# Kernel tuning notes

Measured on AMD Instinct MI355X. Metric: run time of the kernel, lower is better.

The kernel has to match this reference:

```python
import jax, jax.numpy as jnp
import numpy as np

# ---- production-scale dims ----
U, I, D = 51200, 25600, 64          # users, items, embed_size
E, EP = 1_000_000, 100_000          # train edges, pos/neg scoring edges
K = 8                               # topk similar users (FFT filter length)
NF = K // 2 + 1                     # rfft bins
CL_BS = 256                         # contrastive chunk size (U % CL_BS == 0)
TEMP = 0.2                          # args.temperature
N_LAYERS = 2                        # args.layers


def setup_inputs() -> dict:
    key = jax.random.key(0)
    ks = jax.random.split(key, 14)
    return {
        "user_emb": jax.random.normal(ks[0], (U, D), jnp.float32) * 0.1,
        "item_emb": jax.random.normal(ks[1], (I, D), jnp.float32) * 0.1,
        "W": jax.random.normal(ks[2], (D, D), jnp.float32) * (1.0 / np.sqrt(D)),
        "a": jax.random.normal(ks[3], (D,), jnp.float32) * 0.1,
        "WU": jax.random.normal(ks[4], (D, D), jnp.float32) * (1.0 / np.sqrt(D)),
        "aU": jax.random.normal(ks[5], (2 * D,), jnp.float32) * 0.1,
        "complex_weight": jax.random.normal(ks[6], (1, NF, D, 2), jnp.float32) * 0.02,
        "rate_src": jax.random.randint(ks[7], (E,), 0, U),
        "rate_dst": jax.random.randint(ks[8], (E,), 0, I),
        "pos_u": jax.random.randint(ks[9], (EP,), 0, U),
        "pos_i": jax.random.randint(ks[10], (EP,), 0, I),
        "neg_u": jax.random.randint(ks[11], (EP,), 0, U),
        "neg_i": jax.random.randint(ks[12], (EP,), 0, I),
        "nbr_idx": jax.random.randint(ks[13], (U, K), 0, U),
    }


def _propagate(src_feat, src_idx, dst_idx, n_dst):
    """DGRecLayer: degree-normalized mean aggregation over bipartite edges."""
    msg = src_feat[src_idx]                                       # [E, D] gather
    agg = jax.ops.segment_sum(msg, dst_idx, num_segments=n_dst)   # [n_dst, D] scatter
    deg = jax.ops.segment_sum(jnp.ones((src_idx.shape[0],), src_feat.dtype),
                              dst_idx, num_segments=n_dst)
    return agg / jnp.maximum(deg, 1.0)[:, None]


def _layer_attention(ls, W, a):
    t = jnp.stack(ls, axis=0)                                     # [L+1, N, D]
    alpha = jax.nn.softmax(jnp.einsum('lnd,de,e->ln', t, W, a), axis=0)
    return jnp.einsum('lnd,ln->nd', t, alpha)


def _anchor_user_embed(user_emb, WU, aU, complex_weight, nbr_idx):
    # Original detaches user embeddings to numpy for the FAISS path.
    ue = jax.lax.stop_gradient(user_emb)
    simu = ue[nbr_idx]                                            # [U, K, D]
    x = jnp.fft.rfft(simu, axis=1, norm='ortho')                  # [U, NF, D]
    wc = complex_weight[..., 0] + 1j * complex_weight[..., 1]     # [1, NF, D]
    simu = jnp.fft.irfft(x * wc, n=K, axis=1, norm='ortho')       # [U, K, D]
    Wsimu = jnp.einsum('ukd,de->uke', simu, WU)                   # [U, K, D]
    Wu = jnp.broadcast_to((ue @ WU)[:, None, :], Wsimu.shape)     # [U, K, D]
    e = jnp.concatenate([Wsimu, Wu], axis=2) @ aU                 # [U, K]
    e = jnp.where(e > 0, e, 0.1 * e)                              # LeakyReLU(0.1)
    alpha = jax.nn.softmax(e, axis=1)
    return jnp.einsum('uke,uk->ue', Wsimu, alpha)                 # [U, D]


def _chunk_contrast(r1, r2):
    B = r1.shape[0]
    n1 = jnp.linalg.norm(r1, axis=-1, keepdims=True)
    n2 = jnp.linalg.norm(r2, axis=-1, keepdims=True)
    s11 = (r1 @ r1.T) / (n1 @ n1.T + 1e-6) / TEMP
    c12 = (r1 @ r2.T) / (n1 @ n2.T + 1e-6) / TEMP
    s22 = (r2 @ r2.T) / (n2 @ n2.T + 1e-6) / TEMP
    c21 = (r2 @ r1.T) / (n2 @ n1.T + 1e-6) / TEMP
    mask = jax.nn.one_hot(jnp.arange(B), 2 * B, dtype=r1.dtype) * (-1e10)
    logits = jnp.concatenate(
        [jnp.concatenate([s11, c12], axis=-1) + mask,
         jnp.concatenate([s22, c21], axis=-1) + mask], axis=0)     # [2B, 2B]
    labels = jnp.concatenate([jnp.arange(B) + B, jnp.arange(B) + B])
    logz = jax.scipy.special.logsumexp(logits, axis=-1)
    return logz - logits[jnp.arange(2 * B), labels]                # per-example CE


def reference(user_emb, item_emb, W, a, WU, aU, complex_weight,
              rate_src, rate_dst, pos_u, pos_i, neg_u, neg_i, nbr_idx):
    h_u, h_i = user_emb, item_emb
    users, items = [h_u], [h_i]
    for _ in range(N_LAYERS):
        new_i = _propagate(h_u, rate_src, rate_dst, I)   # user -> item ('rate')
        new_u = _propagate(h_i, rate_dst, rate_src, U)   # item -> user ('rated by')
        h_u, h_i = new_u, new_i
        users.append(h_u)
        items.append(h_i)
    hu = _layer_attention(users, W, a)                   # [U, D]
    hi = _layer_attention(items, W, a)                   # [I, D]

    anchor = _anchor_user_embed(user_emb, WU, aU, complex_weight, nbr_idx)
    r1 = hu.reshape(-1, CL_BS, D)
    r2 = anchor.reshape(-1, CL_BS, D)
    loss_contrast = jax.vmap(_chunk_contrast)(r1, r2).mean()

    score_pos = jnp.sum(hu[pos_u] * hi[pos_i], axis=-1, keepdims=True)  # u_dot_v
    score_neg = jnp.sum(hu[neg_u] * hi[neg_i], axis=-1, keepdims=True)
    return score_pos, score_neg, loss_contrast
```

## Files before the change

kernel.cpp:

```cpp
#include <hip/hip_runtime.h>
#include <hip/hip_bf16.h>

constexpr int U_  = 51200;
constexpr int I_  = 25600;
constexpr int E_  = 1000000;
constexpr int EP_ = 100000;
constexpr int CB_ = 256;
constexpr int NCHUNK_ = U_ / CB_;
constexpr size_t UD_ = (size_t)U_ * 64;
constexpr size_t ID_ = (size_t)I_ * 64;
constexpr int NBK_ = 200;
constexpr int CAP_ = 8192;
constexpr int TILE_ = 4096;
constexpr int NBA_ = (E_ + TILE_ - 1) / TILE_;
constexpr int NANC_ = U_ / 16;
constexpr int NCVT_ = (int)((UD_ + ID_) / (8 * 256));
constexpr int NSCB_ = (2 * EP_) / 16;

constexpr float SCALE_E_  = 16.f;
constexpr float ISCALE_E_ = 1.f / 16.f;
constexpr float SCALE_1_  = 64.f;
constexpr float ISCALE_1_ = 1.f / 64.f;

constexpr size_t OFF_LOSS  = 0;
constexpr size_t OFF_FLAG  = 1;
constexpr size_t OFF_CURU  = 8;
constexpr size_t OFF_CURI  = 208;
constexpr size_t OFF_VEC   = 448;
constexpr size_t OFF_ROWU  = 1088;
constexpr size_t OFF_ROWI  = ((OFF_ROWU + U_ + 1 + 63) / 64) * 64;
constexpr size_t OFF_CSRU  = ((OFF_ROWI + I_ + 1 + 63) / 64) * 64;
constexpr size_t OFF_CSRI  = OFF_CSRU + E_;
constexpr size_t OFF_U1    = ((OFF_CSRI + E_ + 63) / 64) * 64;
constexpr size_t OFF_I1    = OFF_U1 + UD_;
constexpr size_t OFF_HU    = OFF_I1 + ID_;
constexpr size_t OFF_HI    = OFF_HU + UD_;
constexpr size_t OFF_ANC   = OFF_HI + ID_;
constexpr size_t OFF_UE8   = OFF_ANC + UD_;
constexpr size_t OFF_IE8   = OFF_UE8 + UD_ / 4;
constexpr size_t OFF_U18   = OFF_IE8 + ID_ / 4;
constexpr size_t OFF_I18   = OFF_U18 + UD_ / 4;

#define DEVI static __device__ __forceinline__

typedef _Float16 h2v __attribute__((ext_vector_type(2)));
typedef _Float16 f16x8 __attribute__((ext_vector_type(8)));
typedef float floatx4 __attribute__((ext_vector_type(4)));
typedef unsigned short u16x8 __attribute__((ext_vector_type(8)));

DEVI float b2f(__hip_bfloat16 x) { return __bfloat162float(x); }

DEVI float bfb2f(unsigned short b) {
  unsigned u = ((unsigned)b) << 16; float f; __builtin_memcpy(&f, &u, 4); return f;
}

DEVI float ldf(const void* p, size_t i, int isf32) {
  if (isf32) return ((const float*)p)[i];
  return b2f(((const __hip_bfloat16*)p)[i]);
}

DEVI float frcp(float x) { return __builtin_amdgcn_rcpf(x); }

DEVI float fexp2(float x) {
#if __has_builtin(__builtin_amdgcn_exp2f)
  return __builtin_amdgcn_exp2f(x);
#else
  return exp2f(x);
#endif
}

DEVI float fp8_dec(unsigned v) {
#if __has_builtin(__builtin_amdgcn_cvt_f32_fp8)
  return __builtin_amdgcn_cvt_f32_fp8(v, 0);
#else
  unsigned b = v & 0xFF;
  if (!(b & 0x78)) return 0.f;
  unsigned short h = (unsigned short)(((b & 0x80) << 8) | (((b & 0x7f) + (8 << 3)) << 7));
  _Float16 hf; __builtin_memcpy(&hf, &h, 2);
  return (float)hf;
#endif
}

#if __has_builtin(__builtin_amdgcn_cvt_f32_fp8)
#define FP8D(w, s) __builtin_amdgcn_cvt_f32_fp8((w), (s))
#else
#define FP8D(w, s) fp8_dec(((w) >> (8 * (s))) & 0xFF)
#endif

DEVI unsigned fp8_enc_pk(float a, float b) {
#if __has_builtin(__builtin_amdgcn_cvt_pk_fp8_f32)
  return __builtin_amdgcn_cvt_pk_fp8_f32(a, b, 0u, false);
#else
  auto enc1 = [](float f) -> unsigned {
    _Float16 hf = (_Float16)f; unsigned short hb; __builtin_memcpy(&hb, &hf, 2);
    int s = hb >> 15, e = (hb >> 10) & 31, m = hb & 1023;
    int e8 = e - 15 + 7;
    int m3 = (m + ((1 << 6) + ((m >> 7) & 1))) >> 7;
    if (m3 > 7) { m3 = 0; e8++; }
    if (e8 <= 0) return (unsigned)(s << 7);
    if (e8 > 15) { e8 = 15; m3 = 6; }
    return (unsigned)((s << 7) | (e8 << 3) | m3);
  };
  return enc1(a) | (enc1(b) << 8);
#endif
}

DEVI int waveInclScan(int v, int lane) {
  #pragma unroll
  for (int off = 1; off < 64; off <<= 1) {
    int t = __shfl_up(v, off, 64);
    if (lane >= off) v += t;
  }
  return v;
}

__global__ void prep_kernel(const unsigned short* __restrict__ ueu,
                            const void* __restrict__ W, const void* __restrict__ a,
                            const void* __restrict__ WU, const void* __restrict__ aU,
                            float* __restrict__ vecs, float* __restrict__ flag,
                            float* __restrict__ ws0) {
  int tid = threadIdx.x;
  for (int i = tid; i < 408; i += 256)
    if (i == 0 || i >= 8) ws0[i] = 0.f;
  if (tid < 64) {
    int cnt = 0;
    for (int i = 0; i < 256; i++) {
      int e = (ueu[i] >> 7) & 0xFF;
      if (e >= 130) cnt++;
    }
    int isf32 = (cnt >= 8);
    if (tid == 0) *flag = isf32 ? 1.0f : 0.0f;
    int d = tid;
    float s = 0.f, t1 = 0.f, t2 = 0.f;
    for (int e = 0; e < 64; e++) {
      s += ldf(W, d * 64 + e, isf32) * ldf(a, e, isf32);
      float wue = ldf(WU, d * 64 + e, isf32);
      t1 += wue * ldf(aU, e, isf32);
      t2 += wue * ldf(aU, 64 + e, isf32);
    }
    vecs[d] = s;
    vecs[64 + d] = t1;
    vecs[128 + d] = t2;
  }
}

struct BktSmem {
  int histU[NBK_], histI[NBK_];
  int loffU[NBK_ + 1], loffI[NBK_ + 1];
  int cbU[NBK_], cbI[NBK_];
  int lcU[NBK_], lcI[NBK_];
  int wsU[4], wsI[4];
  unsigned recsU[TILE_], recsI[TILE_];
};
constexpr int WS_ = 72;
struct AncSmem {
  _Float16 WUt[64 * WS_];
  _Float16 mixS[16 * WS_];
  float invSe[16];
  int nbrS[128];
};
constexpr size_t FSA_SMEM = sizeof(BktSmem) > sizeof(AncSmem) ? sizeof(BktSmem) : sizeof(AncSmem);

DEVI void bucketA_body(char* smemRaw, int blk,
    const int* __restrict__ rs, const int* __restrict__ rd,
    unsigned* __restrict__ bufU, unsigned* __restrict__ bufI,
    int* __restrict__ curU, int* __restrict__ curI) {
  BktSmem& S = *(BktSmem*)smemRaw;
  int tid = threadIdx.x;
  int base = blk * TILE_;
  for (int i = tid; i < NBK_; i += 256) { S.histU[i] = 0; S.histI[i] = 0; }
  __syncthreads();
  int ss[16], dd[16];
  #pragma unroll
  for (int t = 0; t < 16; t++) {
    int e = base + t * 256 + tid;
    bool v = e < E_;
    ss[t] = v ? rs[e] : -1;
    dd[t] = v ? rd[e] : 0;
    if (v) {
      atomicAdd(&S.histU[ss[t] >> 8], 1);
      atomicAdd(&S.histI[dd[t] >> 7], 1);
    }
  }
  __syncthreads();
  if (tid < NBK_) {
    int cU = S.histU[tid];
    S.cbU[tid] = tid * CAP_ + (cU ? atomicAdd(&curU[tid], cU) : 0);
    int cI = S.histI[tid];
    S.cbI[tid] = tid * CAP_ + (cI ? atomicAdd(&curI[tid], cI) : 0);
  }
  int lane = tid & 63, wv = tid >> 6;
  int cvU = (tid < NBK_) ? S.histU[tid] : 0;
  int cvI = (tid < NBK_) ? S.histI[tid] : 0;
  int inU = waveInclScan(cvU, lane);
  int inI = waveInclScan(cvI, lane);
  if (lane == 63) { S.wsU[wv] = inU; S.wsI[wv] = inI; }
  __syncthreads();
  int woU = 0, woI = 0;
  for (int w = 0; w < wv; w++) { woU += S.wsU[w]; woI += S.wsI[w]; }
  if (tid < NBK_) {
    S.loffU[tid] = woU + inU - cvU;
    S.loffI[tid] = woI + inI - cvI;
  }
  if (tid == NBK_ - 1) {
    S.loffU[NBK_] = woU + inU;
    S.loffI[NBK_] = woI + inI;
  }
  __syncthreads();
  if (tid < NBK_) { S.lcU[tid] = S.loffU[tid]; S.lcI[tid] = S.loffI[tid]; }
  __syncthreads();
  #pragma unroll
  for (int t = 0; t < 16; t++) {
    if (ss[t] >= 0) {
      int b = ss[t] >> 8;
      int p = atomicAdd(&S.lcU[b], 1);
      S.recsU[p] = ((unsigned)(ss[t] & 255) << 17) | (unsigned)dd[t];
      b = dd[t] >> 7;
      p = atomicAdd(&S.lcI[b], 1);
      S.recsI[p] = ((unsigned)(dd[t] & 127) << 17) | (unsigned)ss[t];
    }
  }
  __syncthreads();
  int totU = S.loffU[NBK_];
  for (int p = tid; p < totU; p += 256) {
    int lo = 0, hi = NBK_;
    while (hi - lo > 1) { int mid = (lo + hi) >> 1; if (S.loffU[mid] <= p) lo = mid; else hi = mid; }
    bufU[S.cbU[lo] + (p - S.loffU[lo])] = S.recsU[p];
  }
  int totI = S.loffI[NBK_];
  for (int p = tid; p < totI; p += 256) {
    int lo = 0, hi = NBK_;
    while (hi - lo > 1) { int mid = (lo + hi) >> 1; if (S.loffI[mid] <= p) lo = mid; else hi = mid; }
    bufI[S.cbI[lo] + (p - S.loffI[lo])] = S.recsI[p];
  }
}

DEVI void anchor_body(char* smemRaw, int blk,
    const void* __restrict__ ue, const void* __restrict__ WU,
    const void* __restrict__ cw, const float* __restrict__ vecs,
    const int* __restrict__ nbr, float* __restrict__ out, int isf32) {
  AncSmem& S = *(AncSmem*)smemRaw;
  int tid = threadIdx.x;
  int wv = tid >> 6, lane = tid & 63;
  int ublk = blk * 16;

  #pragma unroll
  for (int it = 0; it < 16; it++) {
    int k = it * 4 + wv;
    S.WUt[lane * WS_ + k] = (_Float16)ldf(WU, (size_t)k * 64 + lane, isf32);
  }
  if (tid < 128) S.nbrS[tid] = nbr[ublk * 8 + tid];
  __syncthreads();

  float cw0 = ldf(cw, (0 * 64 + lane) * 2, isf32);
  float w1r = ldf(cw, (1 * 64 + lane) * 2, isf32), w1i = ldf(cw, (1 * 64 + lane) * 2 + 1, isf32);
  float w2r = ldf(cw, (2 * 64 + lane) * 2, isf32), w2i = ldf(cw, (2 * 64 + lane) * 2 + 1, isf32);
  float w3r = ldf(cw, (3 * 64 + lane) * 2, isf32), w3i = ldf(cw, (3 * 64 + lane) * 2 + 1, isf32);
  float cw4 = ldf(cw, (4 * 64 + lane) * 2, isf32);
  float v1 = vecs[64 + lane], v2 = vecs[128 + lane];
  const float c1 = 0.70710678118654752440f;

  bool b3 = (lane & 8) != 0, b4 = (lane & 16) != 0, b5 = (lane & 32) != 0;

  float qv0 = ldf(ue, (size_t)(ublk + wv * 4 + 0) * 64 + lane, isf32) * v2;
  float qv1 = ldf(ue, (size_t)(ublk + wv * 4 + 1) * 64 + lane, isf32) * v2;
  float qv2 = ldf(ue, (size_t)(ublk + wv * 4 + 2) * 64 + lane, isf32) * v2;
  float qv3 = ldf(ue, (size_t)(ublk + wv * 4 + 3) * 64 + lane, isf32) * v2;
  qv0 += __shfl_xor(qv0, 16, 64); qv0 += __shfl_xor(qv0, 32, 64);
  qv1 += __shfl_xor(qv1, 16, 64); qv1 += __shfl_xor(qv1, 32, 64);
  qv2 += __shfl_xor(qv2, 16, 64); qv2 += __shfl_xor(qv2, 32, 64);
  qv3 += __shfl_xor(qv3, 16, 64); qv3 += __shfl_xor(qv3, 32, 64);
  float qs0 = b4 ? qv1 : qv0;
  float qs1 = b4 ? qv3 : qv2;
  float qw = b5 ? qs1 : qs0;
  qw += __shfl_xor(qw, 1, 64); qw += __shfl_xor(qw, 2, 64);
  qw += __shfl_xor(qw, 4, 64); qw += __shfl_xor(qw, 8, 64);

  float xc[8], xn[8];
  #pragma unroll
  for (int k = 0; k < 8; k++)
    xc[k] = ldf(ue, (size_t)S.nbrS[wv * 32 + k] * 64 + lane, isf32);

  for (int u4 = 0; u4 < 4; u4++) {
    int uL = wv * 4 + u4;
    if (u4 < 3) {
      #pragma unroll
      for (int k = 0; k < 8; k++)
        xn[k] = ldf(ue, (size_t)S.nbrS[wv * 32 + (u4 + 1) * 8 + k] * 64 + lane, isf32);
    }
    float sA = xc[1] - xc[3] - xc[5] + xc[7];
    float sB = xc[1] + xc[3] - xc[5] - xc[7];
    float ev = (xc[0] + xc[4]) + (xc[2] + xc[6]);
    float od = (xc[1] + xc[5]) + (xc[3] + xc[7]);
    float d04 = xc[0] - xc[4], d26 = xc[2] - xc[6];
    float X0r = ev + od;
    float X1r = d04 + c1 * sA;
    float X1i = -d26 - c1 * sB;
    float X2r = (xc[0] + xc[4]) - (xc[2] + xc[6]);
    float X2i = -(xc[1] - xc[3] + xc[5] - xc[7]);
    float X3r = d04 - c1 * sA;
    float X3i = d26 - c1 * sB;
    float X4r = ev - od;
    float Zr0 = X0r * cw0;
    float Zr1 = X1r * w1r - X1i * w1i, Zi1 = X1r * w1i + X1i * w1r;
    float Zr2 = X2r * w2r - X2i * w2i, Zi2 = X2r * w2i + X2i * w2r;
    float Zr3 = X3r * w3r - X3i * w3i, Zi3 = X3r * w3i + X3i * w3r;
    float Zr4 = X4r * cw4;
    float eP = Zr0 + Zr4, eM = Zr0 - Zr4;
    float t1 = c1 * (Zr1 - Zr3), t2 = c1 * (Zi1 + Zi3);
    float y[8];
    y[0] = eP + 2.f * (Zr1 + Zr2 + Zr3);
    y[1] = eM + 2.f * (t1 - t2 - Zi2);
    y[2] = eP + 2.f * (-Zi1 - Zr2 + Zi3);
    y[3] = eM + 2.f * (-t1 - t2 + Zi2);
    y[4] = eP + 2.f * (-Zr1 + Zr2 - Zr3);
    y[5] = eM + 2.f * (-t1 + t2 - Zi2);
    y[6] = eP + 2.f * (Zi1 - Zr2 - Zi3);
    y[7] = eM + 2.f * (t1 + t2 + Zi2);
    #pragma unroll
    for (int k = 0; k < 8; k++) y[k] *= 0.125f;

    float p0 = y[0] * v1, p1 = y[1] * v1, p2 = y[2] * v1, p3 = y[3] * v1;
    float p4 = y[4] * v1, p5 = y[5] * v1, p6 = y[6] * v1, p7 = y[7] * v1;
    p0 += __shfl_xor(p0, 8, 64);  p0 += __shfl_xor(p0, 16, 64); p0 += __shfl_xor(p0, 32, 64);
    p1 += __shfl_xor(p1, 8, 64);  p1 += __shfl_xor(p1, 16, 64); p1 += __shfl_xor(p1, 32, 64);
    p2 += __shfl_xor(p2, 8, 64);  p2 += __shfl_xor(p2, 16, 64); p2 += __shfl_xor(p2, 32, 64);
    p3 += __shfl_xor(p3, 8, 64);  p3 += __shfl_xor(p3, 16, 64); p3 += __shfl_xor(p3, 32, 64);
    p4 += __shfl_xor(p4, 8, 64);  p4 += __shfl_xor(p4, 16, 64); p4 += __shfl_xor(p4, 32, 64);
    p5 += __shfl_xor(p5, 8, 64);  p5 += __shfl_xor(p5, 16, 64); p5 += __shfl_xor(p5, 32, 64);
    p6 += __shfl_xor(p6, 8, 64);  p6 += __shfl_xor(p6, 16, 64); p6 += __shfl_xor(p6, 32, 64);
    p7 += __shfl_xor(p7, 8, 64);  p7 += __shfl_xor(p7, 16, 64); p7 += __shfl_xor(p7, 32, 64);
    float a0 = b3 ? p1 : p0;
    float a1 = b3 ? p3 : p2;
    float a2 = b3 ? p5 : p4;
    float a3 = b3 ? p7 : p6;
    float c0 = b4 ? a1 : a0;
    float c1s = b4 ? a3 : a2;
    float w = b5 ? c1s : c0;
    w += __shfl_xor(w, 1, 64); w += __shfl_xor(w, 2, 64); w += __shfl_xor(w, 4, 64);

    float qu = __shfl(qw, u4 * 16, 64);
    float v = w + qu;
    v = v > 0.f ? v : 0.1f * v;
    float m = v;
    m = fmaxf(m, __shfl_xor(m, 8, 64));
    m = fmaxf(m, __shfl_xor(m, 16, 64));
    m = fmaxf(m, __shfl_xor(m, 32, 64));
    float wexp = __expf(v - m);
    float se = wexp;
    se += __shfl_xor(se, 8, 64); se += __shfl_xor(se, 16, 64); se += __shfl_xor(se, 32, 64);
    float mix = 0.f;
    #pragma unroll
    for (int k = 0; k < 8; k++)
      mix += __shfl(wexp, k * 8, 64) * y[k];
    S.mixS[uL * WS_ + lane] = (_Float16)mix;
    if (lane == 0) S.invSe[uL] = frcp(se);
    #pragma unroll
    for (int k = 0; k < 8; k++) xc[k] = xn[k];
  }
  __syncthreads();

  int n = lane & 15, qd = lane >> 4;
  f16x8 A0 = *(const f16x8*)&S.mixS[(lane & 15) * WS_ + qd * 8];
  f16x8 A1 = *(const f16x8*)&S.mixS[(lane & 15) * WS_ + 32 + qd * 8];
  f16x8 B0 = *(const f16x8*)&S.WUt[(wv * 16 + n) * WS_ + qd * 8];
  f16x8 B1 = *(const f16x8*)&S.WUt[(wv * 16 + n) * WS_ + 32 + qd * 8];
  const floatx4 zero = {0.f, 0.f, 0.f, 0.f};
  floatx4 acc = __builtin_amdgcn_mfma_f32_16x16x32_f16(A0, B0, zero, 0, 0, 0);
  acc = __builtin_amdgcn_mfma_f32_16x16x32_f16(A1, B1, acc, 0, 0, 0);
  #pragma unroll
  for (int r = 0; r < 4; r++) {
    int m = qd * 4 + r;
    out[(size_t)(ublk + m) * 64 + wv * 16 + n] = acc[r] * S.invSe[m];
  }
}

DEVI void convert_body(int blk, const void* __restrict__ ue, const void* __restrict__ ie,
                       unsigned char* __restrict__ ue8, unsigned char* __restrict__ ie8,
                       int isf32) {
  size_t t = (size_t)blk * 256 + threadIdx.x;
  const void* src; unsigned* dst; size_t o;
  if (t < UD_ / 8) { src = ue; dst = (unsigned*)ue8; o = t; }
  else             { src = ie; dst = (unsigned*)ie8; o = t - UD_ / 8; }
  float v[8];
  if (isf32) {
    float4 f0 = ((const float4*)src)[2 * o];
    float4 f1 = ((const float4*)src)[2 * o + 1];
    v[0] = f0.x; v[1] = f0.y; v[2] = f0.z; v[3] = f0.w;
    v[4] = f1.x; v[5] = f1.y; v[6] = f1.z; v[7] = f1.w;
  } else {
    u16x8 h = ((const u16x8*)src)[o];
    #pragma unroll
    for (int i = 0; i < 8; i++) v[i] = bfb2f(h[i]);
  }
  unsigned lo = fp8_enc_pk(v[0] * SCALE_E_, v[1] * SCALE_E_) |
                (fp8_enc_pk(v[2] * SCALE_E_, v[3] * SCALE_E_) << 16);
  unsigned hi = fp8_enc_pk(v[4] * SCALE_E_, v[5] * SCALE_E_) |
                (fp8_enc_pk(v[6] * SCALE_E_, v[7] * SCALE_E_) << 16);
  dst[2 * o]     = lo;
  dst[2 * o + 1] = hi;
}

__global__ __launch_bounds__(256) void fusedA_kernel(
    const int* __restrict__ rs, const int* __restrict__ rd,
    unsigned* __restrict__ bufU, unsigned* __restrict__ bufI,
    int* __restrict__ curU, int* __restrict__ curI,
    const void* __restrict__ ue, const void* __restrict__ ie,
    const void* __restrict__ WU, const void* __restrict__ cw,
    const float* __restrict__ vecs, const int* __restrict__ nbr,
    float* __restrict__ anc, unsigned char* __restrict__ ue8,
    unsigned char* __restrict__ ie8, const float* __restrict__ flag) {
  __shared__ __align__(16) char smem[FSA_SMEM];
  if (blockIdx.x < NBA_) {
    bucketA_body(smem, blockIdx.x, rs, rd, bufU, bufI, curU, curI);
  } else if (blockIdx.x < NBA_ + NANC_) {
    anchor_body(smem, blockIdx.x - NBA_, ue, WU, cw, vecs, nbr, anc, *flag > 0.5f);
  } else {
    convert_body(blockIdx.x - NBA_ - NANC_, ue, ie, ue8, ie8, *flag > 0.5f);
  }
}

struct BktBSmem {
  int stage[CAP_];
  int cntk[256], offk[256];
  int exclS[256];
  int wsum[4], wsum2[4];
};

__global__ __launch_bounds__(256) void bucketB_kernel(
    const unsigned* __restrict__ bufU, const unsigned* __restrict__ bufI,
    const int* __restrict__ curU, const int* __restrict__ curI,
    int* __restrict__ rowU, int* __restrict__ rowI,
    int* __restrict__ csrU, int* __restrict__ csrI) {
  __shared__ __align__(16) BktBSmem S;
  int tid = threadIdx.x, b = blockIdx.x;
  int side = b >= NBK_;
  int bb = side ? b - NBK_ : b;
  const unsigned* src = (side ? bufI : bufU) + (size_t)bb * CAP_;
  const int* cur = side ? curI : curU;
  int total = cur[bb];
  int kpb   = side ? 128 : 256;
  int* rowptr = side ? rowI : rowU;
  int* csr    = side ? csrI : csrU;
  if (b == 0 && tid == 0) { rowU[U_] = E_; rowI[I_] = E_; }
  int lane = tid & 63, wv = tid >> 6;
  {
    int v = (tid < NBK_) ? cur[tid] : 0;
    int incl = waveInclScan(v, lane);
    if (lane == 63) S.wsum2[wv] = incl;
    S.cntk[tid] = 0;
    __syncthreads();
    int off = 0;
    for (int w = 0; w < wv; w++) off += S.wsum2[w];
    if (tid < NBK_) S.exclS[tid] = off + incl - v;
    __syncthreads();
  }
  int gbase = S.exclS[bb];
  for (int r = tid; r < total; r += 256) atomicAdd(&S.cntk[src[r] >> 17], 1);
  __syncthreads();
  int cv = (tid < kpb) ? S.cntk[tid] : 0;
  int incl = waveInclScan(cv, lane);
  if (lane == 63) S.wsum[wv] = incl;
  __syncthreads();
  int wvoff = 0;
  for (int w = 0; w < wv; w++) wvoff += S.wsum[w];
  int excl = wvoff + incl - cv;
  if (tid < kpb) {
    S.offk[tid] = excl;
    rowptr[bb * kpb + tid] = gbase + excl;
  }
  __syncthreads();
  for (int r = tid; r < total; r += 256) {
    unsigned rec = src[r];
    int slot = atomicAdd(&S.offk[rec >> 17], 1);
    if (slot < CAP_) S.stage[slot] = (int)(rec & 0x1FFFFu);
  }
  __syncthreads();
  for (int s = tid; s < total; s += 256) csr[gbase + s] = S.stage[s];
}

__global__ __launch_bounds__(256) void agg1_kernel(
    const unsigned char* __restrict__ ue8, const unsigned char* __restrict__ ie8,
    const int* __restrict__ rowU, const int* __restrict__ rowI,
    const int* __restrict__ csrU, const int* __restrict__ csrI,
    __hip_bfloat16* __restrict__ u1, __hip_bfloat16* __restrict__ i1,
    unsigned char* __restrict__ u18, unsigned char* __restrict__ i18) {
  int wv = threadIdx.x >> 6, lane = threadIdx.x & 63;
  int sub = lane >> 4, c16 = lane & 15;
  int side = blockIdx.x >= I_ / 4;
  int blk = side ? blockIdx.x - I_ / 4 : blockIdx.x;
  int r = blk * 4 + wv;
  const int* row = side ? rowU : rowI;
  const int* csr = side ? csrU : csrI;
  const unsigned char* src = side ? ie8 : ue8;
  __hip_bfloat16* out = side ? u1 : i1;
  unsigned char* out8 = side ? u18 : i18;
  int s0 = row[r], s1 = row[r + 1];
  float a4[4] = {0.f, 0.f, 0.f, 0.f};
  int j = s0;
  for (; j + 16 <= s1; j += 16) {
    int e0 = csr[j + sub], e1 = csr[j + 4 + sub];
    int e2 = csr[j + 8 + sub], e3 = csr[j + 12 + sub];
    unsigned w0 = *(const unsigned*)(src + (size_t)e0 * 64 + c16 * 4);
    unsigned w1 = *(const unsigned*)(src + (size_t)e1 * 64 + c16 * 4);
    unsigned w2 = *(const unsigned*)(src + (size_t)e2 * 64 + c16 * 4);
    unsigned w3 = *(const unsigned*)(src + (size_t)e3 * 64 + c16 * 4);
    a4[0] += (FP8D(w0, 0) + FP8D(w1, 0)) + (FP8D(w2, 0) + FP8D(w3, 0));
    a4[1] += (FP8D(w0, 1) + FP8D(w1, 1)) + (FP8D(w2, 1) + FP8D(w3, 1));
    a4[2] += (FP8D(w0, 2) + FP8D(w1, 2)) + (FP8D(w2, 2) + FP8D(w3, 2));
    a4[3] += (FP8D(w0, 3) + FP8D(w1, 3)) + (FP8D(w2, 3) + FP8D(w3, 3));
  }
  if (j + 8 <= s1) {
    int e0 = csr[j + sub], e1 = csr[j + 4 + sub];
    unsigned w0 = *(const unsigned*)(src + (size_t)e0 * 64 + c16 * 4);
    unsigned w1 = *(const unsigned*)(src + (size_t)e1 * 64 + c16 * 4);
    a4[0] += FP8D(w0, 0) + FP8D(w1, 0);
    a4[1] += FP8D(w0, 1) + FP8D(w1, 1);
    a4[2] += FP8D(w0, 2) + FP8D(w1, 2);
    a4[3] += FP8D(w0, 3) + FP8D(w1, 3);
    j += 8;
  }
  if (j + 4 <= s1) {
    int e0 = csr[j + sub];
    unsigned w0 = *(const unsigned*)(src + (size_t)e0 * 64 + c16 * 4);
    a4[0] += FP8D(w0, 0); a4[1] += FP8D(w0, 1);
    a4[2] += FP8D(w0, 2); a4[3] += FP8D(w0, 3);
    j += 4;
  }
  int rem = s1 - j;
  if (sub < rem) {
    int e0 = csr[j + sub];
    unsigned w0 = *(const unsigned*)(src + (size_t)e0 * 64 + c16 * 4);
    a4[0] += FP8D(w0, 0); a4[1] += FP8D(w0, 1);
    a4[2] += FP8D(w0, 2); a4[3] += FP8D(w0, 3);
  }
  #pragma unroll
  for (int c = 0; c < 4; c++) {
    a4[c] += __shfl_xor(a4[c], 16, 64);
    a4[c] += __shfl_xor(a4[c], 32, 64);
  }
  float acc = sub == 0 ? a4[0] : sub == 1 ? a4[1] : sub == 2 ? a4[2] : a4[3];
  int col = c16 * 4 + sub;
  float val = acc * ISCALE_E_ * frcp(fmaxf((float)(s1 - s0), 1.0f));
  size_t idx = (size_t)r * 64 + col;
  out[idx] = __float2bfloat16(val);
  unsigned p = fp8_enc_pk(val * SCALE_1_, val * SCALE_1_);
  out8[idx] = (unsigned char)(p & 0xFF);
}

__global__ __launch_bounds__(256) void agg2attn_kernel(
    const unsigned char* __restrict__ u18, const unsigned char* __restrict__ i18,
    const __hip_bfloat16* __restrict__ u1, const __hip_bfloat16* __restrict__ i1,
    const void* __restrict__ ue, const void* __restrict__ ie,
    const int* __restrict__ rowU, const int* __restrict__ rowI,
    const int* __restrict__ csrU, const int* __restrict__ csrI,
    const float* __restrict__ vecs, float* __restrict__ hu, float* __restrict__ hi,
    const float* __restrict__ flag) {
  int isf32 = *flag > 0.5f;
  int wv = threadIdx.x >> 6, lane = threadIdx.x & 63;
  int sub = lane >> 4, c16 = lane & 15;
  int side = blockIdx.x >= I_ / 4;
  int blk = side ? blockIdx.x - I_ / 4 : blockIdx.x;
  int r = blk * 4 + wv;
  const int* row = side ? rowU : rowI;
  const int* csr = side ? csrU : csrI;
  const unsigned char* opp8 = side ? i18 : u18;
  const __hip_bfloat16* own1 = side ? u1 : i1;
  const void* base = side ? ue : ie;
  float* h = side ? hu : hi;
  int s0 = row[r], s1 = row[r + 1];
  float a4[4] = {0.f, 0.f, 0.f, 0.f};
  int j = s0;
  for (; j + 16 <= s1; j += 16) {
    int e0 = csr[j + sub], e1 = csr[j + 4 + sub];
    int e2 = csr[j + 8 + sub], e3 = csr[j + 12 + sub];
    unsigned w0 = *(const unsigned*)(opp8 + (size_t)e0 * 64 + c16 * 4);
    unsigned w1 = *(const unsigned*)(opp8 + (size_t)e1 * 64 + c16 * 4);
    unsigned w2 = *(const unsigned*)(opp8 + (size_t)e2 * 64 + c16 * 4);
    unsigned w3 = *(const unsigned*)(opp8 + (size_t)e3 * 64 + c16 * 4);
    a4[0] += (FP8D(w0, 0) + FP8D(w1, 0)) + (FP8D(w2, 0) + FP8D(w3, 0));
    a4[1] += (FP8D(w0, 1) + FP8D(w1, 1)) + (FP8D(w2, 1) + FP8D(w3, 1));
    a4[2] += (FP8D(w0, 2) + FP8D(w1, 2)) + (FP8D(w2, 2) + FP8D(w3, 2));
    a4[3] += (FP8D(w0, 3) + FP8D(w1, 3)) + (FP8D(w2, 3) + FP8D(w3, 3));
  }
  if (j + 8 <= s1) {
    int e0 = csr[j + sub], e1 = csr[j + 4 + sub];
    unsigned w0 = *(const unsigned*)(opp8 + (size_t)e0 * 64 + c16 * 4);
    unsigned w1 = *(const unsigned*)(opp8 + (size_t)e1 * 64 + c16 * 4);
    a4[0] += FP8D(w0, 0) + FP8D(w1, 0);
    a4[1] += FP8D(w0, 1) + FP8D(w1, 1);
    a4[2] += FP8D(w0, 2) + FP8D(w1, 2);
    a4[3] += FP8D(w0, 3) + FP8D(w1, 3);
    j += 8;
  }
  if (j + 4 <= s1) {
    int e0 = csr[j + sub];
    unsigned w0 = *(const unsigned*)(opp8 + (size_t)e0 * 64 + c16 * 4);
    a4[0] += FP8D(w0, 0); a4[1] += FP8D(w0, 1);
    a4[2] += FP8D(w0, 2); a4[3] += FP8D(w0, 3);
    j += 4;
  }
  int rem = s1 - j;
  if (sub < rem) {
    int e0 = csr[j + sub];
    unsigned w0 = *(const unsigned*)(opp8 + (size_t)e0 * 64 + c16 * 4);
    a4[0] += FP8D(w0, 0); a4[1] += FP8D(w0, 1);
    a4[2] += FP8D(w0, 2); a4[3] += FP8D(w0, 3);
  }
  #pragma unroll
  for (int c = 0; c < 4; c++) {
    a4[c] += __shfl_xor(a4[c], 16, 64);
    a4[c] += __shfl_xor(a4[c], 32, 64);
  }
  float acc = sub == 0 ? a4[0] : sub == 1 ? a4[1] : sub == 2 ? a4[2] : a4[3];
  int col = c16 * 4 + sub;
  size_t idx = (size_t)r * 64 + col;
  float t2 = acc * ISCALE_1_ * frcp(fmaxf((float)(s1 - s0), 1.0f));
  float t0 = ldf(base, idx, isf32);
  float t1 = b2f(own1[idx]);
  float w = vecs[col];
  float p0 = t0 * w, p1 = t1 * w, p2 = t2 * w;
  #pragma unroll
  for (int off = 32; off; off >>= 1) {
    p0 += __shfl_xor(p0, off, 64);
    p1 += __shfl_xor(p1, off, 64);
    p2 += __shfl_xor(p2, off, 64);
  }
  float m = fmaxf(p0, fmaxf(p1, p2));
  float e0 = __expf(p0 - m), e1 = __expf(p1 - m), e2 = __expf(p2 - m);
  float inv = 1.0f / (e0 + e1 + e2);
  h[idx] = (t0 * e0 + t1 * e1 + t2 * e2) * inv;
}

constexpr int XS_ = 72;
constexpr float SC_  = 2.6857914f;
constexpr float EPS_ = 1e-6f;
constexpr float LN2_ = 0.6931471805599453f;
__global__ __launch_bounds__(1024) void contrast_kernel(
    const float* __restrict__ hu, const float* __restrict__ an,
    float* __restrict__ loss_acc) {
  __shared__ __align__(16) _Float16 Xh[512 * XS_];
  __shared__ float iN[512];
  int tid = threadIdx.x;
  int c = blockIdx.x;

  {
    int rid = tid >> 1, half = tid & 1;
    int row = rid & 255;
    const float* r1 = (rid < 256 ? hu : an) + ((size_t)c * CB_ + row) * 64 + half * 32;
    float4 a4[8];
    float s1 = 0.f;
    #pragma unroll
    for (int t = 0; t < 8; t++) {
      a4[t] = ((const float4*)r1)[t];
      s1 += a4[t].x * a4[t].x + a4[t].y * a4[t].y + a4[t].z * a4[t].z + a4[t].w * a4[t].w;
    }
    s1 += __shfl_xor(s1, 1, 64);
    float inv = frcp(sqrtf(s1));
    if (half == 0) iN[rid] = inv;
    float sc = inv * SC_;
    #pragma unroll
    for (int t = 0; t < 4; t++) {
      f16x8 v;
      v[0] = (_Float16)(a4[2*t].x * sc);   v[1] = (_Float16)(a4[2*t].y * sc);
      v[2] = (_Float16)(a4[2*t].z * sc);   v[3] = (_Float16)(a4[2*t].w * sc);
      v[4] = (_Float16)(a4[2*t+1].x * sc); v[5] = (_Float16)(a4[2*t+1].y * sc);
      v[6] = (_Float16)(a4[2*t+1].z * sc); v[7] = (_Float16)(a4[2*t+1].w * sc);
      *(f16x8*)&Xh[rid * XS_ + half * 32 + t * 8] = v;
    }
  }
  __syncthreads();

  int l = tid & 63, wv = tid >> 6;
  int n = l & 15, q = l >> 4;
  int rb = wv * 32;
  f16x8 A[2][2];
  #pragma unroll
  for (int t = 0; t < 2; t++) {
    A[t][0] = *(const f16x8*)&Xh[(rb + t * 16 + n) * XS_ + q * 8];
    A[t][1] = *(const f16x8*)&Xh[(rb + t * 16 + n) * XS_ + 32 + q * 8];
  }
  float eNiR[2][4];
  #pragma unroll
  for (int t = 0; t < 2; t++)
    #pragma unroll
    for (int r = 0; r < 4; r++)
      eNiR[t][r] = EPS_ * iN[rb + t * 16 + q * 4 + r];
  float sums[2][4] = {{0,0,0,0},{0,0,0,0}};
  float labs2[2] = {0, 0};
  int selfn = q * 4;
  const floatx4 zero = {0.f, 0.f, 0.f, 0.f};
  for (int ct = 0; ct < 32; ct++) {
    f16x8 B0 = *(const f16x8*)&Xh[(ct * 16 + n) * XS_ + q * 8];
    f16x8 B1 = *(const f16x8*)&Xh[(ct * 16 + n) * XS_ + 32 + q * 8];
    float iNj = iN[ct * 16 + n];
    #pragma unroll
    for (int t = 0; t < 2; t++) {
      floatx4 acc = __builtin_amdgcn_mfma_f32_16x16x32_f16(A[t][0], B0, zero, 0, 0, 0);
      acc = __builtin_amdgcn_mfma_f32_16x16x32_f16(A[t][1], B1, acc, 0, 0, 0);
      int rtg = wv * 2 + t;
      if (ct == (rtg ^ 16)) {
        #pragma unroll
        for (int r = 0; r < 4; r++) {
          float G = acc[r];
          float u = eNiR[t][r] * iNj;
          float s2 = __builtin_fmaf(G, -u, G);
          sums[t][r] += fexp2(s2);
          if (n == selfn + r) labs2[t] += s2;
        }
      } else if (ct == rtg) {
        #pragma unroll
        for (int r = 0; r < 4; r++) {
          float G = acc[r];
          float u = eNiR[t][r] * iNj;
          float s2 = __builtin_fmaf(G, -u, G);
          float e = (n == selfn + r) ? 0.f : fexp2(s2);
          sums[t][r] += e;
        }
      } else {
        #pragma unroll
        for (int r = 0; r < 4; r++) {
          float G = acc[r];
          float u = eNiR[t][r] * iNj;
          float s2 = __builtin_fmaf(G, -u, G);
          sums[t][r] += fexp2(s2);
        }
      }
    }
  }
  #pragma unroll
  for (int off = 1; off <= 8; off <<= 1) {
    #pragma unroll
    for (int t = 0; t < 2; t++) {
      #pragma unroll
      for (int r = 0; r < 4; r++) sums[t][r] += __shfl_xor(sums[t][r], off, 64);
      labs2[t] += __shfl_xor(labs2[t], off, 64);
    }
  }
  float part = 0.f;
  if (n == 0) {
    #pragma unroll
    for (int t = 0; t < 2; t++) {
      float lt = 0.f;
      #pragma unroll
      for (int r = 0; r < 4; r++) lt += __logf(sums[t][r]);
      part += lt - labs2[t] * LN2_;
    }
  }
  #pragma unroll
  for (int off = 1; off < 64; off <<= 1) part += __shfl_xor(part, off, 64);
  if (l == 0) atomicAdd(loss_acc, part);
}

__global__ __launch_bounds__(256) void score_kernel(
    const float* __restrict__ hu, const float* __restrict__ hi,
    const int* __restrict__ pu, const int* __restrict__ pi,
    const int* __restrict__ nu, const int* __restrict__ ni,
    void* __restrict__ out, const float* __restrict__ flag,
    const float* __restrict__ loss_acc) {
  int isf32 = *flag > 0.5f;
  if (blockIdx.x == 0 && threadIdx.x == 0) {
    float v = loss_acc[0] * (1.0f / (float)(2 * CB_ * NCHUNK_));
    if (isf32) ((float*)out)[2 * EP_] = v;
    else       ((__hip_bfloat16*)out)[2 * EP_] = __float2bfloat16(v);
  }
  int lane = threadIdx.x & 63;
  int g = lane >> 4, c = lane & 15;
  int gw = blockIdx.x * 4 + (threadIdx.x >> 6);
  int w = gw * 4 + g;
  int uu, ii;
  if (w < EP_) { uu = pu[w]; ii = pi[w]; }
  else         { uu = nu[w - EP_]; ii = ni[w - EP_]; }
  float4 a = *(const float4*)(hu + (size_t)uu * 64 + c * 4);
  float4 b = *(const float4*)(hi + (size_t)ii * 64 + c * 4);
  float p = a.x * b.x + a.y * b.y + a.z * b.z + a.w * b.w;
  #pragma unroll
  for (int off = 1; off < 16; off <<= 1) p += __shfl_xor(p, off, 64);
  if (c == 0) {
    if (isf32) ((float*)out)[w] = p;
    else       ((__hip_bfloat16*)out)[w] = __float2bfloat16(p);
  }
}

extern "C" void kernel_launch(void* const* d_in, const int* in_sizes, int n_in,
                              void* d_out, int out_size, void* d_ws, size_t ws_size,
                              hipStream_t stream) {
  const void* ue  = d_in[0];
  const void* ie  = d_in[1];
  const void* W   = d_in[2];
  const void* a   = d_in[3];
  const void* WU  = d_in[4];
  const void* aU  = d_in[5];
  const void* cw  = d_in[6];
  const int* rs  = (const int*)d_in[7];
  const int* rd  = (const int*)d_in[8];
  const int* pu  = (const int*)d_in[9];
  const int* pi  = (const int*)d_in[10];
  const int* nu  = (const int*)d_in[11];
  const int* ni  = (const int*)d_in[12];
  const int* nbr = (const int*)d_in[13];

  float* wsf  = (float*)d_ws;
  int*   wsi  = (int*)d_ws;
  float* loss = wsf + OFF_LOSS;
  float* flag = wsf + OFF_FLAG;
  int* curU   = wsi + OFF_CURU;
  int* curI   = wsi + OFF_CURI;
  float* vecs = wsf + OFF_VEC;
  int* rowU   = wsi + OFF_ROWU;
  int* rowI   = wsi + OFF_ROWI;
  int* csrU   = wsi + OFF_CSRU;
  int* csrI   = wsi + OFF_CSRI;
  __hip_bfloat16* u1 = (__hip_bfloat16*)(wsf + OFF_U1);
  __hip_bfloat16* i1 = (__hip_bfloat16*)(wsf + OFF_I1);
  float* hu   = wsf + OFF_HU;
  float* hi   = wsf + OFF_HI;
  float* anc  = wsf + OFF_ANC;
  unsigned char* ue8 = (unsigned char*)(wsf + OFF_UE8);
  unsigned char* ie8 = (unsigned char*)(wsf + OFF_IE8);
  unsigned char* u18 = (unsigned char*)(wsf + OFF_U18);
  unsigned char* i18 = (unsigned char*)(wsf + OFF_I18);
  unsigned* bufU = (unsigned*)(wsf + OFF_HU);
  unsigned* bufI = (unsigned*)(wsf + OFF_HI);

  prep_kernel<<<1, 256, 0, stream>>>((const unsigned short*)ue, W, a, WU, aU,
                                     vecs, flag, wsf);

  fusedA_kernel<<<NBA_ + NANC_ + NCVT_, 256, 0, stream>>>(
      rs, rd, bufU, bufI, curU, curI, ue, ie, WU, cw, vecs, nbr, anc, ue8, ie8, flag);

  bucketB_kernel<<<2 * NBK_, 256, 0, stream>>>(bufU, bufI, curU, curI,
                                               rowU, rowI, csrU, csrI);

  agg1_kernel<<<(I_ + U_) / 4, 256, 0, stream>>>(ue8, ie8, rowU, rowI, csrU, csrI,
                                                 u1, i1, u18, i18);
  agg2attn_kernel<<<(I_ + U_) / 4, 256, 0, stream>>>(u18, i18, u1, i1, ue, ie,
                                                     rowU, rowI, csrU, csrI,
                                                     vecs, hu, hi, flag);

  contrast_kernel<<<NCHUNK_, 1024, 0, stream>>>(hu, anc, loss);

  score_kernel<<<NSCB_, 256, 0, stream>>>(hu, hi, pu, pi, nu, ni, d_out, flag, loss);
}
```

Before: 328.9 us.

## Widen fp8 gather loads to 8 bytes and move convert blocks into bucketB

```diff
diff --git a/kernel.cpp b/kernel.cpp
--- a/kernel.cpp
+++ b/kernel.cpp
@@ -122,22 +122,25 @@
   int tid = threadIdx.x;
   for (int i = tid; i < 408; i += 256)
     if (i == 0 || i >= 8) ws0[i] = 0.f;
-  if (tid < 64) {
-    int cnt = 0;
-    for (int i = 0; i < 256; i++) {
-      int e = (ueu[i] >> 7) & 0xFF;
-      if (e >= 130) cnt++;
-    }
-    int isf32 = (cnt >= 8);
-    if (tid == 0) *flag = isf32 ? 1.0f : 0.0f;
-    int d = tid;
-    float s = 0.f, t1 = 0.f, t2 = 0.f;
-    for (int e = 0; e < 64; e++) {
-      s += ldf(W, d * 64 + e, isf32) * ldf(a, e, isf32);
-      float wue = ldf(WU, d * 64 + e, isf32);
-      t1 += wue * ldf(aU, e, isf32);
-      t2 += wue * ldf(aU, 64 + e, isf32);
-    }
+  int cnt = 0;
+  for (int i = 0; i < 256; i++) {
+    int e = (ueu[i] >> 7) & 0xFF;
+    if (e >= 130) cnt++;
+  }
+  int isf32 = (cnt >= 8);
+  if (tid == 0) *flag = isf32 ? 1.0f : 0.0f;
+  int d = tid >> 2, q = tid & 3;
+  float s = 0.f, t1 = 0.f, t2 = 0.f;
+  for (int e = q * 16; e < q * 16 + 16; e++) {
+    s += ldf(W, d * 64 + e, isf32) * ldf(a, e, isf32);
+    float wue = ldf(WU, d * 64 + e, isf32);
+    t1 += wue * ldf(aU, e, isf32);
+    t2 += wue * ldf(aU, 64 + e, isf32);
+  }
+  s  += __shfl_xor(s, 1, 64);  s  += __shfl_xor(s, 2, 64);
+  t1 += __shfl_xor(t1, 1, 64); t1 += __shfl_xor(t1, 2, 64);
+  t2 += __shfl_xor(t2, 1, 64); t2 += __shfl_xor(t2, 2, 64);
+  if (q == 0) {
     vecs[d] = s;
     vecs[64 + d] = t1;
     vecs[128 + d] = t2;
@@ -375,6 +378,22 @@
   }
 }
 
+__global__ __launch_bounds__(256) void fusedA_kernel(
+    const int* __restrict__ rs, const int* __restrict__ rd,
+    unsigned* __restrict__ bufU, unsigned* __restrict__ bufI,
+    int* __restrict__ curU, int* __restrict__ curI,
+    const void* __restrict__ ue,
+    const void* __restrict__ WU, const void* __restrict__ cw,
+    const float* __restrict__ vecs, const int* __restrict__ nbr,
+    float* __restrict__ anc, const float* __restrict__ flag) {
+  __shared__ __align__(16) char smem[FSA_SMEM];
+  if (blockIdx.x < NBA_) {
+    bucketA_body(smem, blockIdx.x, rs, rd, bufU, bufI, curU, curI);
+  } else {
+    anchor_body(smem, blockIdx.x - NBA_, ue, WU, cw, vecs, nbr, anc, *flag > 0.5f);
+  }
+}
+
 DEVI void convert_body(int blk, const void* __restrict__ ue, const void* __restrict__ ie,
                        unsigned char* __restrict__ ue8, unsigned char* __restrict__ ie8,
                        int isf32) {
@@ -401,25 +420,6 @@
   dst[2 * o + 1] = hi;
 }
 
-__global__ __launch_bounds__(256) void fusedA_kernel(
-    const int* __restrict__ rs, const int* __restrict__ rd,
-    unsigned* __restrict__ bufU, unsigned* __restrict__ bufI,
-    int* __restrict__ curU, int* __restrict__ curI,
-    const void* __restrict__ ue, const void* __restrict__ ie,
-    const void* __restrict__ WU, const void* __restrict__ cw,
-    const float* __restrict__ vecs, const int* __restrict__ nbr,
-    float* __restrict__ anc, unsigned char* __restrict__ ue8,
-    unsigned char* __restrict__ ie8, const float* __restrict__ flag) {
-  __shared__ __align__(16) char smem[FSA_SMEM];
-  if (blockIdx.x < NBA_) {
-    bucketA_body(smem, blockIdx.x, rs, rd, bufU, bufI, curU, curI);
-  } else if (blockIdx.x < NBA_ + NANC_) {
-    anchor_body(smem, blockIdx.x - NBA_, ue, WU, cw, vecs, nbr, anc, *flag > 0.5f);
-  } else {
-    convert_body(blockIdx.x - NBA_ - NANC_, ue, ie, ue8, ie8, *flag > 0.5f);
-  }
-}
-
 struct BktBSmem {
   int stage[CAP_];
   int cntk[256], offk[256];
@@ -427,13 +427,13 @@
   int wsum[4], wsum2[4];
 };
 
-__global__ __launch_bounds__(256) void bucketB_kernel(
+DEVI void bucketB_body(char* smemRaw, int b,
     const unsigned* __restrict__ bufU, const unsigned* __restrict__ bufI,
     const int* __restrict__ curU, const int* __restrict__ curI,
     int* __restrict__ rowU, int* __restrict__ rowI,
     int* __restrict__ csrU, int* __restrict__ csrI) {
-  __shared__ __align__(16) BktBSmem S;
-  int tid = threadIdx.x, b = blockIdx.x;
+  BktBSmem& S = *(BktBSmem*)smemRaw;
+  int tid = threadIdx.x;
   int side = b >= NBK_;
   int bb = side ? b - NBK_ : b;
   const unsigned* src = (side ? bufI : bufU) + (size_t)bb * CAP_;
@@ -479,6 +479,22 @@
   for (int s = tid; s < total; s += 256) csr[gbase + s] = S.stage[s];
 }
 
+__global__ __launch_bounds__(256) void bucketB_kernel(
+    const unsigned* __restrict__ bufU, const unsigned* __restrict__ bufI,
+    const int* __restrict__ curU, const int* __restrict__ curI,
+    int* __restrict__ rowU, int* __restrict__ rowI,
+    int* __restrict__ csrU, int* __restrict__ csrI,
+    const void* __restrict__ ue, const void* __restrict__ ie,
+    unsigned char* __restrict__ ue8, unsigned char* __restrict__ ie8,
+    const float* __restrict__ flag) {
+  __shared__ __align__(16) char smem[sizeof(BktBSmem)];
+  if (blockIdx.x < 2 * NBK_) {
+    bucketB_body(smem, blockIdx.x, bufU, bufI, curU, curI, rowU, rowI, csrU, csrI);
+  } else {
+    convert_body(blockIdx.x - 2 * NBK_, ue, ie, ue8, ie8, *flag > 0.5f);
+  }
+}
+
 __global__ __launch_bounds__(256) void agg1_kernel(
     const unsigned char* __restrict__ ue8, const unsigned char* __restrict__ ie8,
     const int* __restrict__ rowU, const int* __restrict__ rowI,
@@ -486,7 +502,7 @@
     __hip_bfloat16* __restrict__ u1, __hip_bfloat16* __restrict__ i1,
     unsigned char* __restrict__ u18, unsigned char* __restrict__ i18) {
   int wv = threadIdx.x >> 6, lane = threadIdx.x & 63;
-  int sub = lane >> 4, c16 = lane & 15;
+  int sub = lane >> 3, c8 = lane & 7;
   int side = blockIdx.x >= I_ / 4;
   int blk = side ? blockIdx.x - I_ / 4 : blockIdx.x;
   int r = blk * 4 + wv;
@@ -496,51 +512,54 @@
   __hip_bfloat16* out = side ? u1 : i1;
   unsigned char* out8 = side ? u18 : i18;
   int s0 = row[r], s1 = row[r + 1];
-  float a4[4] = {0.f, 0.f, 0.f, 0.f};
+  float a8[8] = {0.f, 0.f, 0.f, 0.f, 0.f, 0.f, 0.f, 0.f};
   int j = s0;
   for (; j + 16 <= s1; j += 16) {
-    int e0 = csr[j + sub], e1 = csr[j + 4 + sub];
-    int e2 = csr[j + 8 + sub], e3 = csr[j + 12 + sub];
-    unsigned w0 = *(const unsigned*)(src + (size_t)e0 * 64 + c16 * 4);
-    unsigned w1 = *(const unsigned*)(src + (size_t)e1 * 64 + c16 * 4);
-    unsigned w2 = *(const unsigned*)(src + (size_t)e2 * 64 + c16 * 4);
-    unsigned w3 = *(const unsigned*)(src + (size_t)e3 * 64 + c16 * 4);
-    a4[0] += (FP8D(w0, 0) + FP8D(w1, 0)) + (FP8D(w2, 0) + FP8D(w3, 0));
-    a4[1] += (FP8D(w0, 1) + FP8D(w1, 1)) + (FP8D(w2, 1) + FP8D(w3, 1));
-    a4[2] += (FP8D(w0, 2) + FP8D(w1, 2)) + (FP8D(w2, 2) + FP8D(w3, 2));
-    a4[3] += (FP8D(w0, 3) + FP8D(w1, 3)) + (FP8D(w2, 3) + FP8D(w3, 3));
+    int e0 = csr[j + sub], e1 = csr[j + 8 + sub];
+    uint2 w0 = *(const uint2*)(src + (size_t)e0 * 64 + c8 * 8);
+    uint2 w1 = *(const uint2*)(src + (size_t)e1 * 64 + c8 * 8);
+    a8[0] += FP8D(w0.x, 0) + FP8D(w1.x, 0);
+    a8[1] += FP8D(w0.x, 1) + FP8D(w1.x, 1);
+    a8[2] += FP8D(w0.x, 2) + FP8D(w1.x, 2);
+    a8[3] += FP8D(w0.x, 3) + FP8D(w1.x, 3);
+    a8[4] += FP8D(w0.y, 0) + FP8D(w1.y, 0);
+    a8[5] += FP8D(w0.y, 1) + FP8D(w1.y, 1);
+    a8[6] += FP8D(w0.y, 2) + FP8D(w1.y, 2);
+    a8[7] += FP8D(w0.y, 3) + FP8D(w1.y, 3);
   }
   if (j + 8 <= s1) {
-    int e0 = csr[j + sub], e1 = csr[j + 4 + sub];
-    unsigned w0 = *(const unsigned*)(src + (size_t)e0 * 64 + c16 * 4);
-    unsigned w1 = *(const unsigned*)(src + (size_t)e1 * 64 + c16 * 4);
-    a4[0] += FP8D(w0, 0) + FP8D(w1, 0);
-    a4[1] += FP8D(w0, 1) + FP8D(w1, 1);
-    a4[2] += FP8D(w0, 2) + FP8D(w1, 2);
-    a4[3] += FP8D(w0, 3) + FP8D(w1, 3);
+    int e0 = csr[j + sub];
+    uint2 w0 = *(const uint2*)(src + (size_t)e0 * 64 + c8 * 8);
+    a8[0] += FP8D(w0.x, 0); a8[1] += FP8D(w0.x, 1);
+    a8[2] += FP8D(w0.x, 2); a8[3] += FP8D(w0.x, 3);
+    a8[4] += FP8D(w0.y, 0); a8[5] += FP8D(w0.y, 1);
+    a8[6] += FP8D(w0.y, 2); a8[7] += FP8D(w0.y, 3);
     j += 8;
-  }
-  if (j + 4 <= s1) {
-    int e0 = csr[j + sub];
-    unsigned w0 = *(const unsigned*)(src + (size_t)e0 * 64 + c16 * 4);
-    a4[0] += FP8D(w0, 0); a4[1] += FP8D(w0, 1);
-    a4[2] += FP8D(w0, 2); a4[3] += FP8D(w0, 3);
-    j += 4;
   }
   int rem = s1 - j;
   if (sub < rem) {
     int e0 = csr[j + sub];
-    unsigned w0 = *(const unsigned*)(src + (size_t)e0 * 64 + c16 * 4);
-    a4[0] += FP8D(w0, 0); a4[1] += FP8D(w0, 1);
-    a4[2] += FP8D(w0, 2); a4[3] += FP8D(w0, 3);
-  }
-  #pragma unroll
-  for (int c = 0; c < 4; c++) {
-    a4[c] += __shfl_xor(a4[c], 16, 64);
-    a4[c] += __shfl_xor(a4[c], 32, 64);
-  }
-  float acc = sub == 0 ? a4[0] : sub == 1 ? a4[1] : sub == 2 ? a4[2] : a4[3];
-  int col = c16 * 4 + sub;
+    uint2 w0 = *(const uint2*)(src + (size_t)e0 * 64 + c8 * 8);
+    a8[0] += FP8D(w0.x, 0); a8[1] += FP8D(w0.x, 1);
+    a8[2] += FP8D(w0.x, 2); a8[3] += FP8D(w0.x, 3);
+    a8[4] += FP8D(w0.y, 0); a8[5] += FP8D(w0.y, 1);
+    a8[6] += FP8D(w0.y, 2); a8[7] += FP8D(w0.y, 3);
+  }
+  #pragma unroll
+  for (int c = 0; c < 8; c++) {
+    a8[c] += __shfl_xor(a8[c], 8, 64);
+    a8[c] += __shfl_xor(a8[c], 16, 64);
+    a8[c] += __shfl_xor(a8[c], 32, 64);
+  }
+  bool sb0 = (sub & 1) != 0, sb1 = (sub & 2) != 0, sb2 = (sub & 4) != 0;
+  float x0 = sb0 ? a8[1] : a8[0];
+  float x1 = sb0 ? a8[3] : a8[2];
+  float x2 = sb0 ? a8[5] : a8[4];
+  float x3 = sb0 ? a8[7] : a8[6];
+  float y0 = sb1 ? x1 : x0;
+  float y1 = sb1 ? x3 : x2;
+  float acc = sb2 ? y1 : y0;
+  int col = c8 * 8 + sub;
   float val = acc * ISCALE_E_ * frcp(fmaxf((float)(s1 - s0), 1.0f));
   size_t idx = (size_t)r * 64 + col;
   out[idx] = __float2bfloat16(val);
@@ -558,7 +577,7 @@
     const float* __restrict__ flag) {
   int isf32 = *flag > 0.5f;
   int wv = threadIdx.x >> 6, lane = threadIdx.x & 63;
-  int sub = lane >> 4, c16 = lane & 15;
+  int sub = lane >> 3, c8 = lane & 7;
   int side = blockIdx.x >= I_ / 4;
   int blk = side ? blockIdx.x - I_ / 4 : blockIdx.x;
   int r = blk * 4 + wv;
@@ -569,51 +588,54 @@
   const void* base = side ? ue : ie;
   float* h = side ? hu : hi;
   int s0 = row[r], s1 = row[r + 1];
-  float a4[4] = {0.f, 0.f, 0.f, 0.f};
+  float a8[8] = {0.f, 0.f, 0.f, 0.f, 0.f, 0.f, 0.f, 0.f};
   int j = s0;
   for (; j + 16 <= s1; j += 16) {
-    int e0 = csr[j + sub], e1 = csr[j + 4 + sub];
-    int e2 = csr[j + 8 + sub], e3 = csr[j + 12 + sub];
-    unsigned w0 = *(const unsigned*)(opp8 + (size_t)e0 * 64 + c16 * 4);
-    unsigned w1 = *(const unsigned*)(opp8 + (size_t)e1 * 64 + c16 * 4);
-    unsigned w2 = *(const unsigned*)(opp8 + (size_t)e2 * 64 + c16 * 4);
-    unsigned w3 = *(const unsigned*)(opp8 + (size_t)e3 * 64 + c16 * 4);
-    a4[0] += (FP8D(w0, 0) + FP8D(w1, 0)) + (FP8D(w2, 0) + FP8D(w3, 0));
-    a4[1] += (FP8D(w0, 1) + FP8D(w1, 1)) + (FP8D(w2, 1) + FP8D(w3, 1));
-    a4[2] += (FP8D(w0, 2) + FP8D(w1, 2)) + (FP8D(w2, 2) + FP8D(w3, 2));
-    a4[3] += (FP8D(w0, 3) + FP8D(w1, 3)) + (FP8D(w2, 3) + FP8D(w3, 3));
+    int e0 = csr[j + sub], e1 = csr[j + 8 + sub];
+    uint2 w0 = *(const uint2*)(opp8 + (size_t)e0 * 64 + c8 * 8);
+    uint2 w1 = *(const uint2*)(opp8 + (size_t)e1 * 64 + c8 * 8);
+    a8[0] += FP8D(w0.x, 0) + FP8D(w1.x, 0);
+    a8[1] += FP8D(w0.x, 1) + FP8D(w1.x, 1);
+    a8[2] += FP8D(w0.x, 2) + FP8D(w1.x, 2);
+    a8[3] += FP8D(w0.x, 3) + FP8D(w1.x, 3);
+    a8[4] += FP8D(w0.y, 0) + FP8D(w1.y, 0);
+    a8[5] += FP8D(w0.y, 1) + FP8D(w1.y, 1);
+    a8[6] += FP8D(w0.y, 2) + FP8D(w1.y, 2);
+    a8[7] += FP8D(w0.y, 3) + FP8D(w1.y, 3);
   }
   if (j + 8 <= s1) {
-    int e0 = csr[j + sub], e1 = csr[j + 4 + sub];
-    unsigned w0 = *(const unsigned*)(opp8 + (size_t)e0 * 64 + c16 * 4);
-    unsigned w1 = *(const unsigned*)(opp8 + (size_t)e1 * 64 + c16 * 4);
-    a4[0] += FP8D(w0, 0) + FP8D(w1, 0);
-    a4[1] += FP8D(w0, 1) + FP8D(w1, 1);
-    a4[2] += FP8D(w0, 2) + FP8D(w1, 2);
-    a4[3] += FP8D(w0, 3) + FP8D(w1, 3);
+    int e0 = csr[j + sub];
+    uint2 w0 = *(const uint2*)(opp8 + (size_t)e0 * 64 + c8 * 8);
+    a8[0] += FP8D(w0.x, 0); a8[1] += FP8D(w0.x, 1);
+    a8[2] += FP8D(w0.x, 2); a8[3] += FP8D(w0.x, 3);
+    a8[4] += FP8D(w0.y, 0); a8[5] += FP8D(w0.y, 1);
+    a8[6] += FP8D(w0.y, 2); a8[7] += FP8D(w0.y, 3);
     j += 8;
-  }
-  if (j + 4 <= s1) {
-    int e0 = csr[j + sub];
-    unsigned w0 = *(const unsigned*)(opp8 + (size_t)e0 * 64 + c16 * 4);
-    a4[0] += FP8D(w0, 0); a4[1] += FP8D(w0, 1);
-    a4[2] += FP8D(w0, 2); a4[3] += FP8D(w0, 3);
-    j += 4;
   }
   int rem = s1 - j;
   if (sub < rem) {
     int e0 = csr[j + sub];
-    unsigned w0 = *(const unsigned*)(opp8 + (size_t)e0 * 64 + c16 * 4);
-    a4[0] += FP8D(w0, 0); a4[1] += FP8D(w0, 1);
-    a4[2] += FP8D(w0, 2); a4[3] += FP8D(w0, 3);
-  }
-  #pragma unroll
-  for (int c = 0; c < 4; c++) {
-    a4[c] += __shfl_xor(a4[c], 16, 64);
-    a4[c] += __shfl_xor(a4[c], 32, 64);
-  }
-  float acc = sub == 0 ? a4[0] : sub == 1 ? a4[1] : sub == 2 ? a4[2] : a4[3];
-  int col = c16 * 4 + sub;
+    uint2 w0 = *(const uint2*)(opp8 + (size_t)e0 * 64 + c8 * 8);
+    a8[0] += FP8D(w0.x, 0); a8[1] += FP8D(w0.x, 1);
+    a8[2] += FP8D(w0.x, 2); a8[3] += FP8D(w0.x, 3);
+    a8[4] += FP8D(w0.y, 0); a8[5] += FP8D(w0.y, 1);
+    a8[6] += FP8D(w0.y, 2); a8[7] += FP8D(w0.y, 3);
+  }
+  #pragma unroll
+  for (int c = 0; c < 8; c++) {
+    a8[c] += __shfl_xor(a8[c], 8, 64);
+    a8[c] += __shfl_xor(a8[c], 16, 64);
+    a8[c] += __shfl_xor(a8[c], 32, 64);
+  }
+  bool sb0 = (sub & 1) != 0, sb1 = (sub & 2) != 0, sb2 = (sub & 4) != 0;
+  float x0 = sb0 ? a8[1] : a8[0];
+  float x1 = sb0 ? a8[3] : a8[2];
+  float x2 = sb0 ? a8[5] : a8[4];
+  float x3 = sb0 ? a8[7] : a8[6];
+  float y0 = sb1 ? x1 : x0;
+  float y1 = sb1 ? x3 : x2;
+  float acc = sb2 ? y1 : y0;
+  int col = c8 * 8 + sub;
   size_t idx = (size_t)r * 64 + col;
   float t2 = acc * ISCALE_1_ * frcp(fmaxf((float)(s1 - s0), 1.0f));
   float t0 = ldf(base, idx, isf32);
@@ -826,11 +848,11 @@
   prep_kernel<<<1, 256, 0, stream>>>((const unsigned short*)ue, W, a, WU, aU,
                                      vecs, flag, wsf);
 
-  fusedA_kernel<<<NBA_ + NANC_ + NCVT_, 256, 0, stream>>>(
-      rs, rd, bufU, bufI, curU, curI, ue, ie, WU, cw, vecs, nbr, anc, ue8, ie8, flag);
-
-  bucketB_kernel<<<2 * NBK_, 256, 0, stream>>>(bufU, bufI, curU, curI,
-                                               rowU, rowI, csrU, csrI);
+  fusedA_kernel<<<NBA_ + NANC_, 256, 0, stream>>>(
+      rs, rd, bufU, bufI, curU, curI, ue, WU, cw, vecs, nbr, anc, flag);
+
+  bucketB_kernel<<<2 * NBK_ + NCVT_, 256, 0, stream>>>(
+      bufU, bufI, curU, curI, rowU, rowI, csrU, csrI, ue, ie, ue8, ie8, flag);
 
   agg1_kernel<<<(I_ + U_) / 4, 256, 0, stream>>>(ue8, ie8, rowU, rowI, csrU, csrI,
                                                  u1, i1, u18, i18);
```

Measured after the change: 327.1 us, median of 2. Within noise of the previous version (-0.6%).
